# Kernel tuning notes

Hardware: AMD Instinct MI355X
Metric: run time of the kernel (lower is better)

Reference implementation:

```python
import jax, jax.numpy as jnp
import numpy as np

E = 6            # number of residual adapter experts / event groups
MAX_SCALE = 0.05
RESIDUAL_SCALE = 1.0
EPS = 1e-12      # F.normalize eps


def setup_inputs() -> dict:
    key = jax.random.key(0)
    ks = jax.random.split(key, 8)
    B, L, D, H, T = 4, 1024, 768, 1536, 32
    seq_embeddings = jax.random.normal(ks[0], (B, L, D), dtype=jnp.float32)
    next_type_ids = jax.random.randint(ks[1], (B, L), 0, T, dtype=jnp.int32)
    # Adapter bank params (6 two-layer MLPs). Original zero-inits W2/b2; we use
    # small random values so the math is exercised.
    W1 = jax.random.normal(ks[2], (E, D, H), dtype=jnp.float32) * 0.02
    b1 = jax.random.normal(ks[3], (E, H), dtype=jnp.float32) * 0.02
    W2 = jax.random.normal(ks[4], (E, H, D), dtype=jnp.float32) * 0.02
    b2 = jax.random.normal(ks[5], (E, D), dtype=jnp.float32) * 0.02
    raw_alpha = jnp.full((E,), -4.0, dtype=jnp.float32)
    # build_event_type_to_group_tensor stand-in: event type -> one of 6 groups
    event_type_to_group = (jnp.arange(T, dtype=jnp.int32) % E)
    return {"seq_embeddings": seq_embeddings, "next_type_ids": next_type_ids,
            "W1": W1, "b1": b1, "W2": W2, "b2": b2,
            "raw_alpha": raw_alpha, "event_type_to_group": event_type_to_group}


def reference(seq_embeddings, next_type_ids, W1, b1, W2, b2, raw_alpha, event_type_to_group):
    x = seq_embeddings                                  # [B, L, D]
    T = event_type_to_group.shape[0]
    safe = jnp.clip(next_type_ids.astype(jnp.int32), 0, T - 1)
    group_ids = event_type_to_group[safe]               # [B, L] in [0, 6)
    # Dense compute of all 6 adapters (dropout is identity in eval mode)
    h = jax.nn.relu(jnp.einsum('bld,edh->bleh', x, W1) + b1)   # [B, L, 6, H]
    residuals = jnp.einsum('bleh,ehd->bled', h, W2) + b2       # [B, L, 6, D]
    # Gather the chosen expert's residual per token
    idx = group_ids[..., None, None]                           # [B, L, 1, 1]
    residual = jnp.take_along_axis(residuals, idx, axis=2)[:, :, 0, :]  # [B, L, D]
    alpha_all = MAX_SCALE * jax.nn.sigmoid(raw_alpha)          # [6]
    alpha = alpha_all[group_ids][..., None]                    # [B, L, 1]
    out = x + RESIDUAL_SCALE * alpha * residual
    norm = jnp.linalg.norm(out, axis=-1, keepdims=True)
    out = out / jnp.maximum(norm, EPS)
    return out
```

## Files before the change

kernel.cpp:

```cpp
#include <hip/hip_runtime.h>
#include <hip/hip_bf16.h>
#include <stdint.h>

#define NTOK 4096
#define DDIM 768
#define HDIM 1536
#define NEXP 6
#define NTYPE 32
#define PADROWS 4224

typedef __bf16 bf16x8 __attribute__((ext_vector_type(8)));
typedef float f32x4 __attribute__((ext_vector_type(4)));

static __device__ __forceinline__ unsigned short f2bf(float f) {
  union { float f; unsigned u; } v; v.f = f;
  unsigned r = v.u + 0x7FFFu + ((v.u >> 16) & 1u);
  return (unsigned short)(r >> 16);
}

static __device__ __forceinline__ void gload_lds16(const void* g, void* lds) {
  auto* g1 = reinterpret_cast<const __attribute__((address_space(1))) uint32_t*>(
      reinterpret_cast<uintptr_t>(g));
  auto* l3 = reinterpret_cast<__attribute__((address_space(3))) uint32_t*>(
      (uint32_t)reinterpret_cast<uintptr_t>(lds));
  __builtin_amdgcn_global_load_lds(g1, l3, 16, 0, 0);
}

__global__ __launch_bounds__(256)
void prep_kernel(const float* __restrict__ W1, const float* __restrict__ W2,
                 unsigned short* __restrict__ w1t, unsigned short* __restrict__ w2t,
                 const int* __restrict__ ids, const int* __restrict__ ev2g,
                 int* __restrict__ perm, int* __restrict__ meta) {
  const int z = blockIdx.z;
  const int t = threadIdx.x;
  if (z == 12) {
    if (blockIdx.x != 0 || blockIdx.y != 0) return;
    __shared__ int s_ev2g[NTYPE];
    __shared__ int s_cnt[NEXP];
    __shared__ int s_off[NEXP];
    __shared__ int s_cur[NEXP];
    if (t < NTYPE) s_ev2g[t] = ev2g[t];
    if (t < NEXP) { s_cnt[t] = 0; s_cur[t] = 0; }
    __syncthreads();
    int g[16];
    #pragma unroll
    for (int i = 0; i < 16; ++i) {
      int idx = t * 16 + i;
      int ty = ids[idx];
      ty = ty < 0 ? 0 : (ty > NTYPE - 1 ? NTYPE - 1 : ty);
      g[i] = s_ev2g[ty];
      atomicAdd(&s_cnt[g[i]], 1);
    }
    __syncthreads();
    if (t == 0) {
      int off = 0, nt = 0;
      int* table = meta + 21;
      for (int e = 0; e < NEXP; ++e) {
        s_off[e] = off;
        int c = s_cnt[e];
        for (int k = 0; k * 128 < c; ++k) {
          int rem = c - k * 128;
          table[nt * 3 + 0] = e;
          table[nt * 3 + 1] = off + k * 128;
          table[nt * 3 + 2] = rem < 128 ? rem : 128;
          ++nt;
        }
        off += c;
      }
      meta[20] = nt;
    }
    __syncthreads();
    #pragma unroll
    for (int i = 0; i < 16; ++i) {
      int idx = t * 16 + i;
      int pos = s_off[g[i]] + atomicAdd(&s_cur[g[i]], 1);
      perm[pos] = idx;
    }
    return;
  }
  __shared__ float tile[64][65];
  const float* src;
  unsigned short* dst;
  int R, C, bx, by;
  if (z < 6) {
    src = W1 + (size_t)z * 768 * 1536; dst = w1t + (size_t)z * 768 * 1536;
    R = 768; C = 1536; bx = blockIdx.x; by = blockIdx.y;
  } else {
    src = W2 + (size_t)(z - 6) * 768 * 1536; dst = w2t + (size_t)(z - 6) * 768 * 1536;
    R = 1536; C = 768; bx = blockIdx.y; by = blockIdx.x;
  }
  const int r0 = by * 64, c0 = bx * 64;
  const int lr = t >> 4;
  const int lc = (t & 15) << 2;
  #pragma unroll
  for (int i = 0; i < 4; ++i) {
    float4 v = *reinterpret_cast<const float4*>(src + (size_t)(r0 + i * 16 + lr) * C + c0 + lc);
    tile[i * 16 + lr][lc]     = v.x;
    tile[i * 16 + lr][lc + 1] = v.y;
    tile[i * 16 + lr][lc + 2] = v.z;
    tile[i * 16 + lr][lc + 3] = v.w;
  }
  __syncthreads();
  const int l8 = (t & 7) << 3;
  #pragma unroll
  for (int p = 0; p < 2; ++p) {
    int j = p * 32 + (t >> 3);
    union { unsigned short u[8]; uint4 v; } pk;
    #pragma unroll
    for (int k = 0; k < 8; ++k) pk.u[k] = f2bf(tile[l8 + k][j]);
    *reinterpret_cast<uint4*>(dst + (size_t)(c0 + j) * R + r0 + l8) = pk.v;
  }
}

__global__ __launch_bounds__(256)
void xgather_kernel(const float* __restrict__ x, const int* __restrict__ perm,
                    unsigned short* __restrict__ xg) {
  const int wave = threadIdx.x >> 6, lane = threadIdx.x & 63;
  const int row = (blockIdx.x << 2) + wave;
  const int src = perm[row];
  const float4* in = reinterpret_cast<const float4*>(x + (size_t)src * DDIM);
  ushort4* outp = reinterpret_cast<ushort4*>(xg + (size_t)row * DDIM);
  #pragma unroll
  for (int j = 0; j < 3; ++j) {
    float4 v = in[lane + j * 64];
    ushort4 o;
    o.x = f2bf(v.x); o.y = f2bf(v.y); o.z = f2bf(v.z); o.w = f2bf(v.w);
    outp[lane + j * 64] = o;
  }
}

template <int K, int NT, bool PASS2>
__global__ __launch_bounds__(256, 2)
void gemm_kernel(const unsigned short* __restrict__ A,
                 const unsigned short* __restrict__ Bw,
                 const float* __restrict__ bias,
                 const int* __restrict__ meta,
                 const int* __restrict__ perm,
                 const float* __restrict__ x,
                 const float* __restrict__ raw_alpha,
                 unsigned short* __restrict__ hout,
                 float* __restrict__ out)
{
  constexpr int BM = 128, BN = 128;
  constexpr int NDIM = NT * BN;
  constexpr int NK = K / 64;

  const int nwg = 40 * NT;
  const int q = nwg >> 3;
  const int vid = (blockIdx.x & 7) * q + (blockIdx.x >> 3);
  const int nt = vid / 40;
  const int mt = vid % 40;
  if (mt >= meta[20]) return;
  const int* table = meta + 21;
  const int e = table[mt * 3 + 0], base = table[mt * 3 + 1], cnt = table[mt * 3 + 2];

  __shared__ __align__(16) unsigned short As[2][BM * 64];
  __shared__ __align__(16) unsigned short Bs[2][BN * 64];

  const int tid = threadIdx.x;
  const int wave = tid >> 6, lane = tid & 63;
  const int wm = wave >> 1, wn = wave & 1;

  const unsigned short* Abase = A + (size_t)base * K;
  const unsigned short* Bbase = Bw + ((size_t)e * NDIM + (size_t)nt * BN) * K;

  f32x4 acc[4][4];
  #pragma unroll
  for (int i = 0; i < 4; ++i)
    #pragma unroll
    for (int j = 0; j < 4; ++j) acc[i][j] = (f32x4){0.f, 0.f, 0.f, 0.f};

  int sRow[4], sElem[4], sLds[4];
  #pragma unroll
  for (int i = 0; i < 4; ++i) {
    int chunk = i * 256 + tid;
    int o = chunk * 16;
    int row = o >> 7;
    int inb = (o & 127) ^ ((row & 7) << 4);
    sRow[i] = row; sElem[i] = inb >> 1;
    sLds[i] = (i * 256 + wave * 64) * 16;
  }

  #pragma unroll
  for (int i = 0; i < 4; ++i)
    gload_lds16(Abase + (size_t)sRow[i] * K + sElem[i], (char*)As[0] + sLds[i]);
  #pragma unroll
  for (int i = 0; i < 4; ++i)
    gload_lds16(Bbase + (size_t)sRow[i] * K + sElem[i], (char*)Bs[0] + sLds[i]);
  __syncthreads();

  int cur = 0;
  for (int kt = 0; kt < NK; ++kt) {
    if (kt + 1 < NK) {
      const int k0 = (kt + 1) * 64;
      #pragma unroll
      for (int i = 0; i < 4; ++i)
        gload_lds16(Abase + (size_t)sRow[i] * K + k0 + sElem[i], (char*)As[cur ^ 1] + sLds[i]);
      #pragma unroll
      for (int i = 0; i < 4; ++i)
        gload_lds16(Bbase + (size_t)sRow[i] * K + k0 + sElem[i], (char*)Bs[cur ^ 1] + sLds[i]);
    }
    #pragma unroll
    for (int ks = 0; ks < 2; ++ks) {
      bf16x8 av[4], bv[4];
      const int kb = ks * 64 + ((lane >> 4) << 4);
      #pragma unroll
      for (int mi = 0; mi < 4; ++mi) {
        int row = wm * 64 + mi * 16 + (lane & 15);
        int byte = (row * 128 + kb) ^ ((row & 7) << 4);
        av[mi] = *reinterpret_cast<const bf16x8*>((const char*)As[cur] + byte);
      }
      #pragma unroll
      for (int nj = 0; nj < 4; ++nj) {
        int row = wn * 64 + nj * 16 + (lane & 15);
        int byte = (row * 128 + kb) ^ ((row & 7) << 4);
        bv[nj] = *reinterpret_cast<const bf16x8*>((const char*)Bs[cur] + byte);
      }
      #pragma unroll
      for (int mi = 0; mi < 4; ++mi)
        #pragma unroll
        for (int nj = 0; nj < 4; ++nj)
          acc[mi][nj] = __builtin_amdgcn_mfma_f32_16x16x32_bf16(av[mi], bv[nj], acc[mi][nj], 0, 0, 0);
    }
    __syncthreads();
    cur ^= 1;
  }

  const int col0 = nt * BN + wn * 64;
  if constexpr (!PASS2) {
    #pragma unroll
    for (int nj = 0; nj < 4; ++nj) {
      int n = col0 + nj * 16 + (lane & 15);
      float bv = bias[e * NDIM + n];
      #pragma unroll
      for (int mi = 0; mi < 4; ++mi) {
        int rbase = wm * 64 + mi * 16 + ((lane >> 4) << 2);
        #pragma unroll
        for (int r = 0; r < 4; ++r) {
          int row = rbase + r;
          if (row < cnt) {
            float v = fmaxf(acc[mi][nj][r] + bv, 0.0f);
            hout[(size_t)(base + row) * NDIM + n] = f2bf(v);
          }
        }
      }
    }
  } else {
    float alpha = 0.05f / (1.0f + expf(-raw_alpha[e]));
    #pragma unroll
    for (int nj = 0; nj < 4; ++nj) {
      int n = col0 + nj * 16 + (lane & 15);
      float bv = bias[e * NDIM + n];
      #pragma unroll
      for (int mi = 0; mi < 4; ++mi) {
        int rbase = wm * 64 + mi * 16 + ((lane >> 4) << 2);
        #pragma unroll
        for (int r = 0; r < 4; ++r) {
          int row = rbase + r;
          if (row < cnt) {
            int tok = perm[base + row];
            size_t oi = (size_t)tok * DDIM + n;
            out[oi] = x[oi] + alpha * (acc[mi][nj][r] + bv);
          }
        }
      }
    }
  }
}

__global__ __launch_bounds__(256)
void norm_kernel(float* __restrict__ out) {
  const int wave = threadIdx.x >> 6, lane = threadIdx.x & 63;
  const int tok = (blockIdx.x << 2) + wave;
  float4* p = reinterpret_cast<float4*>(out) + (size_t)tok * 192;
  float4 a = p[lane], b = p[lane + 64], c = p[lane + 128];
  float ss = a.x * a.x + a.y * a.y + a.z * a.z + a.w * a.w
           + b.x * b.x + b.y * b.y + b.z * b.z + b.w * b.w
           + c.x * c.x + c.y * c.y + c.z * c.z + c.w * c.w;
  #pragma unroll
  for (int off = 32; off; off >>= 1) ss += __shfl_xor(ss, off);
  const float s = 1.0f / fmaxf(sqrtf(ss), 1e-12f);
  a.x *= s; a.y *= s; a.z *= s; a.w *= s;
  b.x *= s; b.y *= s; b.z *= s; b.w *= s;
  c.x *= s; c.y *= s; c.z *= s; c.w *= s;
  p[lane] = a; p[lane + 64] = b; p[lane + 128] = c;
}


extern "C" void kernel_launch(void* const* d_in, const int* in_sizes, int n_in,
                              void* d_out, int out_size, void* d_ws, size_t ws_size,
                              hipStream_t stream) {
  const float* x      = (const float*)d_in[0];
  const int*   ids    = (const int*)d_in[1];
  const float* W1     = (const float*)d_in[2];
  const float* b1     = (const float*)d_in[3];
  const float* W2     = (const float*)d_in[4];
  const float* b2     = (const float*)d_in[5];
  const float* ralpha = (const float*)d_in[6];
  const int*   ev2g   = (const int*)d_in[7];
  float* out = (float*)d_out;
  char* ws = (char*)d_ws;

  unsigned short* w1t = (unsigned short*)(ws);
  unsigned short* w2t = (unsigned short*)(ws + 14155776);
  unsigned short* xg  = (unsigned short*)(ws + 28311552);
  unsigned short* h   = (unsigned short*)(ws + 34799616);
  int* perm = (int*)(ws + 47775744);
  int* meta = (int*)(ws + 47808512);

  prep_kernel<<<dim3(24, 12, 13), 256, 0, stream>>>(W1, W2, w1t, w2t, ids, ev2g, perm, meta);
  xgather_kernel<<<1024, 256, 0, stream>>>(x, perm, xg);
  gemm_kernel<DDIM, 12, false><<<480, 256, 0, stream>>>(
      xg, w1t, b1, meta, perm, x, ralpha, h, out);
  gemm_kernel<HDIM, 6, true><<<240, 256, 0, stream>>>(
      h, w2t, b2, meta, perm, x, ralpha, nullptr, out);
  norm_kernel<<<1024, 256, 0, stream>>>(out);
}
```

Baseline: 193.8 us.

## Fuse all stages into one persistent cooperative kernel with grid syncs

Replaces the five separate launches (weight transpose/cast, routing, x cast, two grouped GEMMs, normalization) with one cooperative persistent kernel that loops over task lists and separates phases with grid-wide syncs. The x cast no longer gathers rows; instead the first GEMM gathers A rows through perm pointers. GEMM tiles now use 512 threads with 8 waves, each holding a 64x32 sub-tile. This removes launch gaps and tail idle time between kernels, but adds grid-barrier cost and depends on the occupancy query to size the grid so all blocks are co-resident.

```diff
diff --git a/kernel.cpp b/kernel.cpp
--- a/kernel.cpp
+++ b/kernel.cpp
@@ -1,6 +1,9 @@
 #include <hip/hip_runtime.h>
+#include <hip/hip_cooperative_groups.h>
 #include <hip/hip_bf16.h>
 #include <stdint.h>
+
+namespace cg = cooperative_groups;
 
 #define NTOK 4096
 #define DDIM 768
@@ -8,6 +11,7 @@
 #define NEXP 6
 #define NTYPE 32
 #define PADROWS 4224
+#define MAXT 38
 
 typedef __bf16 bf16x8 __attribute__((ext_vector_type(8)));
 typedef float f32x4 __attribute__((ext_vector_type(4)));
@@ -26,241 +30,129 @@
   __builtin_amdgcn_global_load_lds(g1, l3, 16, 0, 0);
 }
 
-__global__ __launch_bounds__(256)
-void prep_kernel(const float* __restrict__ W1, const float* __restrict__ W2,
-                 unsigned short* __restrict__ w1t, unsigned short* __restrict__ w2t,
-                 const int* __restrict__ ids, const int* __restrict__ ev2g,
-                 int* __restrict__ perm, int* __restrict__ meta) {
-  const int z = blockIdx.z;
-  const int t = threadIdx.x;
-  if (z == 12) {
-    if (blockIdx.x != 0 || blockIdx.y != 0) return;
-    __shared__ int s_ev2g[NTYPE];
-    __shared__ int s_cnt[NEXP];
-    __shared__ int s_off[NEXP];
-    __shared__ int s_cur[NEXP];
-    if (t < NTYPE) s_ev2g[t] = ev2g[t];
-    if (t < NEXP) { s_cnt[t] = 0; s_cur[t] = 0; }
-    __syncthreads();
-    int g[16];
-    #pragma unroll
-    for (int i = 0; i < 16; ++i) {
-      int idx = t * 16 + i;
-      int ty = ids[idx];
-      ty = ty < 0 ? 0 : (ty > NTYPE - 1 ? NTYPE - 1 : ty);
-      g[i] = s_ev2g[ty];
-      atomicAdd(&s_cnt[g[i]], 1);
-    }
-    __syncthreads();
-    if (t == 0) {
-      int off = 0, nt = 0;
-      int* table = meta + 21;
-      for (int e = 0; e < NEXP; ++e) {
-        s_off[e] = off;
-        int c = s_cnt[e];
-        for (int k = 0; k * 128 < c; ++k) {
-          int rem = c - k * 128;
-          table[nt * 3 + 0] = e;
-          table[nt * 3 + 1] = off + k * 128;
-          table[nt * 3 + 2] = rem < 128 ? rem : 128;
-          ++nt;
-        }
-        off += c;
-      }
-      meta[20] = nt;
-    }
-    __syncthreads();
-    #pragma unroll
-    for (int i = 0; i < 16; ++i) {
-      int idx = t * 16 + i;
-      int pos = s_off[g[i]] + atomicAdd(&s_cur[g[i]], 1);
-      perm[pos] = idx;
-    }
-    return;
-  }
-  __shared__ float tile[64][65];
-  const float* src;
-  unsigned short* dst;
-  int R, C, bx, by;
-  if (z < 6) {
-    src = W1 + (size_t)z * 768 * 1536; dst = w1t + (size_t)z * 768 * 1536;
-    R = 768; C = 1536; bx = blockIdx.x; by = blockIdx.y;
-  } else {
-    src = W2 + (size_t)(z - 6) * 768 * 1536; dst = w2t + (size_t)(z - 6) * 768 * 1536;
-    R = 1536; C = 768; bx = blockIdx.y; by = blockIdx.x;
-  }
-  const int r0 = by * 64, c0 = bx * 64;
-  const int lr = t >> 4;
-  const int lc = (t & 15) << 2;
-  #pragma unroll
-  for (int i = 0; i < 4; ++i) {
-    float4 v = *reinterpret_cast<const float4*>(src + (size_t)(r0 + i * 16 + lr) * C + c0 + lc);
-    tile[i * 16 + lr][lc]     = v.x;
-    tile[i * 16 + lr][lc + 1] = v.y;
-    tile[i * 16 + lr][lc + 2] = v.z;
-    tile[i * 16 + lr][lc + 3] = v.w;
-  }
-  __syncthreads();
-  const int l8 = (t & 7) << 3;
-  #pragma unroll
-  for (int p = 0; p < 2; ++p) {
-    int j = p * 32 + (t >> 3);
-    union { unsigned short u[8]; uint4 v; } pk;
-    #pragma unroll
-    for (int k = 0; k < 8; ++k) pk.u[k] = f2bf(tile[l8 + k][j]);
-    *reinterpret_cast<uint4*>(dst + (size_t)(c0 + j) * R + r0 + l8) = pk.v;
-  }
-}
-
-__global__ __launch_bounds__(256)
-void xgather_kernel(const float* __restrict__ x, const int* __restrict__ perm,
-                    unsigned short* __restrict__ xg) {
-  const int wave = threadIdx.x >> 6, lane = threadIdx.x & 63;
-  const int row = (blockIdx.x << 2) + wave;
-  const int src = perm[row];
-  const float4* in = reinterpret_cast<const float4*>(x + (size_t)src * DDIM);
-  ushort4* outp = reinterpret_cast<ushort4*>(xg + (size_t)row * DDIM);
-  #pragma unroll
-  for (int j = 0; j < 3; ++j) {
-    float4 v = in[lane + j * 64];
-    ushort4 o;
-    o.x = f2bf(v.x); o.y = f2bf(v.y); o.z = f2bf(v.z); o.w = f2bf(v.w);
-    outp[lane + j * 64] = o;
-  }
-}
-
-template <int K, int NT, bool PASS2>
-__global__ __launch_bounds__(256, 2)
-void gemm_kernel(const unsigned short* __restrict__ A,
-                 const unsigned short* __restrict__ Bw,
-                 const float* __restrict__ bias,
-                 const int* __restrict__ meta,
-                 const int* __restrict__ perm,
-                 const float* __restrict__ x,
-                 const float* __restrict__ raw_alpha,
-                 unsigned short* __restrict__ hout,
-                 float* __restrict__ out)
+union SMem {
+  struct { unsigned short A[2][128 * 64]; unsigned short B[2][128 * 64]; } g;
+  float tr[64][65];
+  struct { int ev2g[NTYPE]; int cnt[NEXP]; int off[NEXP]; int cur[NEXP]; } bk;
+};
+
+template <int K, int NDIM, bool PASS2>
+static __device__ __forceinline__ void gemm_tile(
+    SMem& sm, int tid, int wave, int lane,
+    const unsigned short* __restrict__ Asrc,
+    const unsigned short* __restrict__ Bw,
+    const float* __restrict__ bias,
+    const int* __restrict__ perm,
+    const float* __restrict__ x,
+    const float* __restrict__ ralpha,
+    unsigned short* __restrict__ hout,
+    float* __restrict__ out,
+    int e, int base, int cnt, int nt)
 {
-  constexpr int BM = 128, BN = 128;
-  constexpr int NDIM = NT * BN;
   constexpr int NK = K / 64;
-
-  const int nwg = 40 * NT;
-  const int q = nwg >> 3;
-  const int vid = (blockIdx.x & 7) * q + (blockIdx.x >> 3);
-  const int nt = vid / 40;
-  const int mt = vid % 40;
-  if (mt >= meta[20]) return;
-  const int* table = meta + 21;
-  const int e = table[mt * 3 + 0], base = table[mt * 3 + 1], cnt = table[mt * 3 + 2];
-
-  __shared__ __align__(16) unsigned short As[2][BM * 64];
-  __shared__ __align__(16) unsigned short Bs[2][BN * 64];
-
-  const int tid = threadIdx.x;
-  const int wave = tid >> 6, lane = tid & 63;
-  const int wm = wave >> 1, wn = wave & 1;
-
-  const unsigned short* Abase = A + (size_t)base * K;
-  const unsigned short* Bbase = Bw + ((size_t)e * NDIM + (size_t)nt * BN) * K;
-
-  f32x4 acc[4][4];
+  const int wm = wave >> 2, wn = wave & 3;
+
+  const unsigned short* Bbase = Bw + ((size_t)e * NDIM + (size_t)nt * 128) * K;
+
+  f32x4 acc[4][2];
   #pragma unroll
   for (int i = 0; i < 4; ++i)
     #pragma unroll
-    for (int j = 0; j < 4; ++j) acc[i][j] = (f32x4){0.f, 0.f, 0.f, 0.f};
-
-  int sRow[4], sElem[4], sLds[4];
+    for (int j = 0; j < 2; ++j) acc[i][j] = (f32x4){0.f, 0.f, 0.f, 0.f};
+
+  int rRow[2], rElem[2], rLds[2];
+  const unsigned short* aRowPtr[2];
   #pragma unroll
-  for (int i = 0; i < 4; ++i) {
-    int chunk = i * 256 + tid;
+  for (int i = 0; i < 2; ++i) {
+    int chunk = i * 512 + tid;
     int o = chunk * 16;
     int row = o >> 7;
     int inb = (o & 127) ^ ((row & 7) << 4);
-    sRow[i] = row; sElem[i] = inb >> 1;
-    sLds[i] = (i * 256 + wave * 64) * 16;
-  }
-
-  #pragma unroll
-  for (int i = 0; i < 4; ++i)
-    gload_lds16(Abase + (size_t)sRow[i] * K + sElem[i], (char*)As[0] + sLds[i]);
-  #pragma unroll
-  for (int i = 0; i < 4; ++i)
-    gload_lds16(Bbase + (size_t)sRow[i] * K + sElem[i], (char*)Bs[0] + sLds[i]);
+    rRow[i] = row; rElem[i] = inb >> 1;
+    rLds[i] = (i * 512 + wave * 64) * 16;
+    int grow;
+    if (PASS2) { grow = base + row; }
+    else { int t = base + row; if (t > NTOK - 1) t = NTOK - 1; grow = perm[t]; }
+    aRowPtr[i] = Asrc + (size_t)grow * K;
+  }
+
+  auto stage = [&](int kt, int buf) {
+    const int k0 = kt * 64;
+    #pragma unroll
+    for (int i = 0; i < 2; ++i)
+      gload_lds16(aRowPtr[i] + k0 + rElem[i], (char*)sm.g.A[buf] + rLds[i]);
+    #pragma unroll
+    for (int i = 0; i < 2; ++i)
+      gload_lds16(Bbase + (size_t)rRow[i] * K + k0 + rElem[i], (char*)sm.g.B[buf] + rLds[i]);
+  };
+
+  stage(0, 0);
   __syncthreads();
 
   int cur = 0;
   for (int kt = 0; kt < NK; ++kt) {
-    if (kt + 1 < NK) {
-      const int k0 = (kt + 1) * 64;
-      #pragma unroll
-      for (int i = 0; i < 4; ++i)
-        gload_lds16(Abase + (size_t)sRow[i] * K + k0 + sElem[i], (char*)As[cur ^ 1] + sLds[i]);
-      #pragma unroll
-      for (int i = 0; i < 4; ++i)
-        gload_lds16(Bbase + (size_t)sRow[i] * K + k0 + sElem[i], (char*)Bs[cur ^ 1] + sLds[i]);
-    }
+    if (kt + 1 < NK) stage(kt + 1, cur ^ 1);
     #pragma unroll
     for (int ks = 0; ks < 2; ++ks) {
-      bf16x8 av[4], bv[4];
+      bf16x8 av[4], bv[2];
       const int kb = ks * 64 + ((lane >> 4) << 4);
       #pragma unroll
       for (int mi = 0; mi < 4; ++mi) {
         int row = wm * 64 + mi * 16 + (lane & 15);
         int byte = (row * 128 + kb) ^ ((row & 7) << 4);
-        av[mi] = *reinterpret_cast<const bf16x8*>((const char*)As[cur] + byte);
-      }
-      #pragma unroll
-      for (int nj = 0; nj < 4; ++nj) {
-        int row = wn * 64 + nj * 16 + (lane & 15);
+        av[mi] = *reinterpret_cast<const bf16x8*>((const char*)sm.g.A[cur] + byte);
+      }
+      #pragma unroll
+      for (int nj = 0; nj < 2; ++nj) {
+        int row = wn * 32 + nj * 16 + (lane & 15);
         int byte = (row * 128 + kb) ^ ((row & 7) << 4);
-        bv[nj] = *reinterpret_cast<const bf16x8*>((const char*)Bs[cur] + byte);
+        bv[nj] = *reinterpret_cast<const bf16x8*>((const char*)sm.g.B[cur] + byte);
       }
       #pragma unroll
       for (int mi = 0; mi < 4; ++mi)
         #pragma unroll
-        for (int nj = 0; nj < 4; ++nj)
+        for (int nj = 0; nj < 2; ++nj)
           acc[mi][nj] = __builtin_amdgcn_mfma_f32_16x16x32_bf16(av[mi], bv[nj], acc[mi][nj], 0, 0, 0);
     }
     __syncthreads();
     cur ^= 1;
   }
 
-  const int col0 = nt * BN + wn * 64;
+  const int col0 = nt * 128 + wn * 32;
   if constexpr (!PASS2) {
     #pragma unroll
-    for (int nj = 0; nj < 4; ++nj) {
+    for (int nj = 0; nj < 2; ++nj) {
       int n = col0 + nj * 16 + (lane & 15);
       float bv = bias[e * NDIM + n];
       #pragma unroll
       for (int mi = 0; mi < 4; ++mi) {
         int rbase = wm * 64 + mi * 16 + ((lane >> 4) << 2);
         #pragma unroll
-        for (int r = 0; r < 4; ++r) {
-          int row = rbase + r;
+        for (int rr = 0; rr < 4; ++rr) {
+          int row = rbase + rr;
           if (row < cnt) {
-            float v = fmaxf(acc[mi][nj][r] + bv, 0.0f);
+            float v = fmaxf(acc[mi][nj][rr] + bv, 0.0f);
             hout[(size_t)(base + row) * NDIM + n] = f2bf(v);
           }
         }
       }
     }
   } else {
-    float alpha = 0.05f / (1.0f + expf(-raw_alpha[e]));
-    #pragma unroll
-    for (int nj = 0; nj < 4; ++nj) {
+    float alpha = 0.05f / (1.0f + expf(-ralpha[e]));
+    #pragma unroll
+    for (int nj = 0; nj < 2; ++nj) {
       int n = col0 + nj * 16 + (lane & 15);
       float bv = bias[e * NDIM + n];
       #pragma unroll
       for (int mi = 0; mi < 4; ++mi) {
         int rbase = wm * 64 + mi * 16 + ((lane >> 4) << 2);
         #pragma unroll
-        for (int r = 0; r < 4; ++r) {
-          int row = rbase + r;
+        for (int rr = 0; rr < 4; ++rr) {
+          int row = rbase + rr;
           if (row < cnt) {
             int tok = perm[base + row];
             size_t oi = (size_t)tok * DDIM + n;
-            out[oi] = x[oi] + alpha * (acc[mi][nj][r] + bv);
+            out[oi] = x[oi] + alpha * (acc[mi][nj][rr] + bv);
           }
         }
       }
@@ -268,22 +160,147 @@
   }
 }
 
-__global__ __launch_bounds__(256)
-void norm_kernel(float* __restrict__ out) {
-  const int wave = threadIdx.x >> 6, lane = threadIdx.x & 63;
-  const int tok = (blockIdx.x << 2) + wave;
-  float4* p = reinterpret_cast<float4*>(out) + (size_t)tok * 192;
-  float4 a = p[lane], b = p[lane + 64], c = p[lane + 128];
-  float ss = a.x * a.x + a.y * a.y + a.z * a.z + a.w * a.w
-           + b.x * b.x + b.y * b.y + b.z * b.z + b.w * b.w
-           + c.x * c.x + c.y * c.y + c.z * c.z + c.w * c.w;
-  #pragma unroll
-  for (int off = 32; off; off >>= 1) ss += __shfl_xor(ss, off);
-  const float s = 1.0f / fmaxf(sqrtf(ss), 1e-12f);
-  a.x *= s; a.y *= s; a.z *= s; a.w *= s;
-  b.x *= s; b.y *= s; b.z *= s; b.w *= s;
-  c.x *= s; c.y *= s; c.z *= s; c.w *= s;
-  p[lane] = a; p[lane + 64] = b; p[lane + 128] = c;
+__global__ __launch_bounds__(512, 4)
+void mega_kernel(const float* __restrict__ x, const int* __restrict__ ids,
+                 const float* __restrict__ W1, const float* __restrict__ b1,
+                 const float* __restrict__ W2, const float* __restrict__ b2,
+                 const float* __restrict__ ralpha, const int* __restrict__ ev2g,
+                 float* __restrict__ out,
+                 unsigned short* __restrict__ w1t, unsigned short* __restrict__ w2t,
+                 unsigned short* __restrict__ xg, unsigned short* __restrict__ h,
+                 int* __restrict__ perm, int* __restrict__ meta)
+{
+  __shared__ SMem sm;
+  cg::grid_group grid = cg::this_grid();
+  const int NB = gridDim.x;
+  const int bid = blockIdx.x;
+  const int tid = threadIdx.x;
+  const int wave = tid >> 6, lane = tid & 63;
+
+  for (int task = bid; task < 3521; task += NB) {
+    if (task < 3456) {
+      const int mat = task / 288;
+      const int t2 = task % 288;
+      const float* src; unsigned short* dst; int R, C, bx, by;
+      if (mat < 6) {
+        src = W1 + (size_t)mat * 768 * 1536; dst = w1t + (size_t)mat * 768 * 1536;
+        R = 768; C = 1536; bx = t2 % 24; by = t2 / 24;
+      } else {
+        src = W2 + (size_t)(mat - 6) * 768 * 1536; dst = w2t + (size_t)(mat - 6) * 768 * 1536;
+        R = 1536; C = 768; bx = t2 % 12; by = t2 / 12;
+      }
+      const int r0 = by * 64, c0 = bx * 64;
+      const int lc = (tid & 15) << 2;
+      #pragma unroll
+      for (int i = 0; i < 2; ++i) {
+        int row = i * 32 + (tid >> 4);
+        float4 v = *reinterpret_cast<const float4*>(src + (size_t)(r0 + row) * C + c0 + lc);
+        sm.tr[row][lc] = v.x; sm.tr[row][lc + 1] = v.y;
+        sm.tr[row][lc + 2] = v.z; sm.tr[row][lc + 3] = v.w;
+      }
+      __syncthreads();
+      const int j = tid >> 3, l8 = (tid & 7) << 3;
+      union { unsigned short u[8]; uint4 v; } pk;
+      #pragma unroll
+      for (int k = 0; k < 8; ++k) pk.u[k] = f2bf(sm.tr[l8 + k][j]);
+      *reinterpret_cast<uint4*>(dst + (size_t)(c0 + j) * R + r0 + l8) = pk.v;
+      __syncthreads();
+    } else if (task == 3456) {
+      if (tid < NTYPE) sm.bk.ev2g[tid] = ev2g[tid];
+      if (tid < NEXP) { sm.bk.cnt[tid] = 0; sm.bk.cur[tid] = 0; }
+      __syncthreads();
+      int g[8];
+      #pragma unroll
+      for (int i = 0; i < 8; ++i) {
+        int idx = tid * 8 + i;
+        int ty = ids[idx];
+        ty = ty < 0 ? 0 : (ty > NTYPE - 1 ? NTYPE - 1 : ty);
+        g[i] = sm.bk.ev2g[ty];
+        atomicAdd(&sm.bk.cnt[g[i]], 1);
+      }
+      __syncthreads();
+      if (tid == 0) {
+        int off = 0, ntl = 0;
+        int* table = meta + 21;
+        for (int e = 0; e < NEXP; ++e) {
+          sm.bk.off[e] = off;
+          int c = sm.bk.cnt[e];
+          for (int k = 0; k * 128 < c; ++k) {
+            int rem = c - k * 128;
+            table[ntl * 3 + 0] = e;
+            table[ntl * 3 + 1] = off + k * 128;
+            table[ntl * 3 + 2] = rem < 128 ? rem : 128;
+            ++ntl;
+          }
+          off += c;
+        }
+        meta[20] = ntl;
+      }
+      __syncthreads();
+      #pragma unroll
+      for (int i = 0; i < 8; ++i) {
+        int idx = tid * 8 + i;
+        int pos = sm.bk.off[g[i]] + atomicAdd(&sm.bk.cur[g[i]], 1);
+        perm[pos] = idx;
+      }
+    } else {
+      const int R0 = (task - 3457) * 64 + wave * 8;
+      #pragma unroll
+      for (int rr = 0; rr < 8; ++rr) {
+        const int row = R0 + rr;
+        const float4* in = reinterpret_cast<const float4*>(x + (size_t)row * DDIM);
+        ushort4* op = reinterpret_cast<ushort4*>(xg + (size_t)row * DDIM);
+        #pragma unroll
+        for (int j = 0; j < 3; ++j) {
+          float4 v = in[lane + j * 64];
+          ushort4 o;
+          o.x = f2bf(v.x); o.y = f2bf(v.y); o.z = f2bf(v.z); o.w = f2bf(v.w);
+          op[lane + j * 64] = o;
+        }
+      }
+    }
+  }
+
+  __threadfence();
+  grid.sync();
+
+  const int ntiles = *(volatile int*)(meta + 20);
+  const int* table = meta + 21;
+  for (int task = bid; task < ntiles * 12; task += NB) {
+    const int nt = task / ntiles, mt = task % ntiles;
+    const int e = table[mt * 3 + 0], base = table[mt * 3 + 1], cnt = table[mt * 3 + 2];
+    gemm_tile<DDIM, HDIM, false>(sm, tid, wave, lane, xg, w1t, b1, perm, x, ralpha,
+                                 h, out, e, base, cnt, nt);
+  }
+
+  __threadfence();
+  grid.sync();
+
+  for (int task = bid; task < ntiles * 6; task += NB) {
+    const int nt = task / ntiles, mt = task % ntiles;
+    const int e = table[mt * 3 + 0], base = table[mt * 3 + 1], cnt = table[mt * 3 + 2];
+    gemm_tile<HDIM, DDIM, true>(sm, tid, wave, lane, h, w2t, b2, perm, x, ralpha,
+                                nullptr, out, e, base, cnt, nt);
+  }
+
+  __threadfence();
+  grid.sync();
+
+  for (int task = bid; task < 512; task += NB) {
+    const int tok = task * 8 + wave;
+    float4* p = reinterpret_cast<float4*>(out) + (size_t)tok * 192;
+    float4 a = p[lane], b = p[lane + 64], c = p[lane + 128];
+    float ss = a.x * a.x + a.y * a.y + a.z * a.z + a.w * a.w
+             + b.x * b.x + b.y * b.y + b.z * b.z + b.w * b.w
+             + c.x * c.x + c.y * c.y + c.z * c.z + c.w * c.w;
+    #pragma unroll
+    for (int off = 32; off; off >>= 1) ss += __shfl_xor(ss, off);
+    const float s = 1.0f / fmaxf(sqrtf(ss), 1e-12f);
+    a.x *= s; a.y *= s; a.z *= s; a.w *= s;
+    b.x *= s; b.y *= s; b.z *= s; b.w *= s;
+    c.x *= s; c.y *= s; c.z *= s; c.w *= s;
+    p[lane] = a; p[lane + 64] = b; p[lane + 128] = c;
+  }
 }
 
 
@@ -308,11 +325,15 @@
   int* perm = (int*)(ws + 47775744);
   int* meta = (int*)(ws + 47808512);
 
-  prep_kernel<<<dim3(24, 12, 13), 256, 0, stream>>>(W1, W2, w1t, w2t, ids, ev2g, perm, meta);
-  xgather_kernel<<<1024, 256, 0, stream>>>(x, perm, xg);
-  gemm_kernel<DDIM, 12, false><<<480, 256, 0, stream>>>(
-      xg, w1t, b1, meta, perm, x, ralpha, h, out);
-  gemm_kernel<HDIM, 6, true><<<240, 256, 0, stream>>>(
-      h, w2t, b2, meta, perm, x, ralpha, nullptr, out);
-  norm_kernel<<<1024, 256, 0, stream>>>(out);
-}
+  int nb = 0;
+  if (hipOccupancyMaxActiveBlocksPerMultiprocessor(&nb, mega_kernel, 512, 0) != hipSuccess || nb < 1)
+    nb = 1;
+  const int grid = nb >= 2 ? 512 : 256;
+
+  void* args[] = {
+    (void*)&x, (void*)&ids, (void*)&W1, (void*)&b1, (void*)&W2, (void*)&b2,
+    (void*)&ralpha, (void*)&ev2g, (void*)&out,
+    (void*)&w1t, (void*)&w2t, (void*)&xg, (void*)&h, (void*)&perm, (void*)&meta
+  };
+  hipLaunchCooperativeKernel(mega_kernel, dim3(grid), dim3(512), args, 0, stream);
+}
```

Measured after the change: 542.3 us. 180% more time.
